# Optimization experiments

Measured on AMD Instinct MI355X. Metric: run time of the kernel, lower is better.

## Reference

```python
import jax, jax.numpy as jnp
import numpy as np

H = 64  # hidden size (fixed by module)

def _gru_cell(x, h, Wih, Whh, bih, bhh):
    # PyTorch GRU cell: gates ordered (r, z, n)
    gi = x @ Wih.T + bih            # [B, 3H]
    gh = h @ Whh.T + bhh            # [B, 3H]
    ir, iz, inn = jnp.split(gi, 3, axis=-1)
    hr, hz, hn = jnp.split(gh, 3, axis=-1)
    r = jax.nn.sigmoid(ir + hr)
    z = jax.nn.sigmoid(iz + hz)
    n = jnp.tanh(inn + r * hn)
    return (1.0 - z) * n + z * h


def setup_inputs() -> dict:
    key = jax.random.key(0)
    ks = jax.random.split(key, 24)
    B, T, NI = 16384, 256, 6
    s = 1.0 / np.sqrt(H)  # torch default GRU init scale
    f32 = jnp.float32
    u = lambda k, shp: jax.random.uniform(k, shp, dtype=f32, minval=-s, maxval=s)
    inp = {
        "x": jax.random.normal(ks[0], (B, T, NI), dtype=f32),
        "target_len": 180,
        # encoder GRU, layer 0 (input size NI) and layer 1 (input size H)
        "e_Wih0": u(ks[1], (3 * H, NI)), "e_Whh0": u(ks[2], (3 * H, H)),
        "e_bih0": u(ks[3], (3 * H,)),    "e_bhh0": u(ks[4], (3 * H,)),
        "e_Wih1": u(ks[5], (3 * H, H)),  "e_Whh1": u(ks[6], (3 * H, H)),
        "e_bih1": u(ks[7], (3 * H,)),    "e_bhh1": u(ks[8], (3 * H,)),
        # decoder GRU, layer 0 (input size 1) and layer 1 (input size H)
        "d_Wih0": u(ks[9], (3 * H, 1)),  "d_Whh0": u(ks[10], (3 * H, H)),
        "d_bih0": u(ks[11], (3 * H,)),   "d_bhh0": u(ks[12], (3 * H,)),
        "d_Wih1": u(ks[13], (3 * H, H)), "d_Whh1": u(ks[14], (3 * H, H)),
        "d_bih1": u(ks[15], (3 * H,)),   "d_bhh1": u(ks[16], (3 * H,)),
        # heads
        "W_on": u(ks[17], (1, H)), "b_on": u(ks[18], (1,)),
        "W_cv": u(ks[19], (1, H)), "b_cv": u(ks[20], (1,)),
    }
    return inp


def reference(x, target_len,
              e_Wih0, e_Whh0, e_bih0, e_bhh0, e_Wih1, e_Whh1, e_bih1, e_bhh1,
              d_Wih0, d_Whh0, d_bih0, d_bhh0, d_Wih1, d_Whh1, d_bih1, d_bhh1,
              W_on, b_on, W_cv, b_cv):
    B = x.shape[0]
    on_threshold = 0.5

    # ---- encoder: 2-layer GRU over the input sequence, keep final hidden ----
    def enc_step(carry, xt):
        h0, h1 = carry
        h0 = _gru_cell(xt, h0, e_Wih0, e_Whh0, e_bih0, e_bhh0)
        h1 = _gru_cell(h0, h1, e_Wih1, e_Whh1, e_bih1, e_bhh1)
        return (h0, h1), None

    h_init = (jnp.zeros((B, H), x.dtype), jnp.zeros((B, H), x.dtype))
    (h0, h1), _ = jax.lax.scan(enc_step, h_init, jnp.swapaxes(x, 0, 1))  # [T,B,NI]

    def dec_step(carry, _):
        prev, h0, h1 = carry                                   # prev: [B,1]
        h0 = _gru_cell(prev, h0, d_Wih0, d_Whh0, d_bih0, d_bhh0)
        h1 = _gru_cell(h0, h1, d_Wih1, d_Whh1, d_bih1, d_bhh1)
        cv = h1 @ W_cv.T + b_cv                                # [B,1]
        logit = h1 @ W_on.T + b_on                             # [B,1]
        gated = (jax.nn.sigmoid(logit) > on_threshold).astype(cv.dtype) * cv
        return (gated, h0, h1), gated

    prev0 = jnp.zeros((B, 1), x.dtype)
    _, outs = jax.lax.scan(dec_step, (prev0, h0, h1), None, length=target_len)
    # outs: [target_len, B, 1] -> [B, target_len, 1] (torch.cat along dim=1)
    return jnp.swapaxes(outs, 0, 1)
```

## Files before the change

### kernel.cpp

```cpp
#include <hip/hip_runtime.h>
#include <math.h>

#define TENC 256
#define NIE  6
#define LH   68
#define WSTR 68

__shared__ float sW1[192 * WSTR];
__shared__ float sU1[192 * WSTR];
__shared__ float sHd[132];
__shared__ float sh0[2][64 * LH];
__shared__ float sh1[64 * LH];

__device__ __forceinline__ float sigm_(float x) {
    return __builtin_amdgcn_rcpf(1.0f + __expf(-x));
}
__device__ __forceinline__ float tanh_(float x) {
    float t = __expf(2.0f * x);
    return (t - 1.0f) * __builtin_amdgcn_rcpf(t + 1.0f);
}

__device__ __forceinline__ void fma4(float& acc, const float4& a, const float4& b) {
    acc = fmaf(a.x, b.x, acc);
    acc = fmaf(a.y, b.y, acc);
    acc = fmaf(a.z, b.z, acc);
    acc = fmaf(a.w, b.w, acc);
}

__device__ __forceinline__ void stage_w1(const float* __restrict__ W1,
                                         const float* __restrict__ U1) {
    for (int s = threadIdx.x; s < 12288; s += 512) {
        int k = s & 63, row = s >> 6;
        int g = row >> 6, j = row & 63;
        int d = (j * 3 + g) * WSTR + k;
        sW1[d] = W1[s];
        sU1[d] = U1[s];
    }
}

template<int KIN>
__device__ __forceinline__ void layer0_c(const float* __restrict__ U0,
                                         const float* w0r, const float* w0z,
                                         const float* w0n,
                                         const float* xin,
                                         const float* b_r, const float* b_z,
                                         const float* b_nx, const float* b_nh,
                                         int jB, int bl,
                                         const float* __restrict__ hb,
                                         float hn[2][4])
{
    float ar[2][4], az[2][4], anx[2][4], anh[2][4];
#pragma unroll
    for (int g = 0; g < 4; ++g) {
#pragma unroll
        for (int jj = 0; jj < 2; ++jj) {
            ar[jj][g] = b_r[jj]; az[jj][g] = b_z[jj];
            anx[jj][g] = b_nx[jj]; anh[jj][g] = b_nh[jj];
        }
    }
#pragma unroll
    for (int jj = 0; jj < 2; ++jj)
#pragma unroll
        for (int g = 0; g < 4; ++g)
#pragma unroll
            for (int k = 0; k < KIN; ++k) {
                ar[jj][g]  = fmaf(w0r[jj * KIN + k], xin[g * KIN + k], ar[jj][g]);
                az[jj][g]  = fmaf(w0z[jj * KIN + k], xin[g * KIN + k], az[jj][g]);
                anx[jj][g] = fmaf(w0n[jj * KIN + k], xin[g * KIN + k], anx[jj][g]);
            }
    const float* u0 = U0 + (size_t)jB * 64;
    const float* u1 = U0 + (size_t)(jB + 1) * 64;
    const float* hr0 = hb + bl * LH;
#pragma unroll 2
    for (int kc = 0; kc < 64; kc += 4) {
        float4 hv[4];
#pragma unroll
        for (int g = 0; g < 4; ++g)
            hv[g] = *(const float4*)(hr0 + g * (16 * LH) + kc);
        float4 r0 = *(const float4*)(u0 + kc);
        float4 z0 = *(const float4*)(u0 + 4096 + kc);
        float4 n0 = *(const float4*)(u0 + 8192 + kc);
        float4 r1 = *(const float4*)(u1 + kc);
        float4 z1 = *(const float4*)(u1 + 4096 + kc);
        float4 n1 = *(const float4*)(u1 + 8192 + kc);
#pragma unroll
        for (int g = 0; g < 4; ++g) {
            fma4(ar[0][g], r0, hv[g]); fma4(az[0][g], z0, hv[g]); fma4(anh[0][g], n0, hv[g]);
            fma4(ar[1][g], r1, hv[g]); fma4(az[1][g], z1, hv[g]); fma4(anh[1][g], n1, hv[g]);
        }
    }
#pragma unroll
    for (int g = 0; g < 4; ++g) {
        float2 ho = *(const float2*)(hb + (bl + 16 * g) * LH + jB);
        float hold[2] = {ho.x, ho.y};
#pragma unroll
        for (int jj = 0; jj < 2; ++jj) {
            float r = sigm_(ar[jj][g]);
            float z = sigm_(az[jj][g]);
            float n = tanh_(fmaf(r, anh[jj][g], anx[jj][g]));
            hn[jj][g] = fmaf(z, hold[jj] - n, n);
        }
    }
}

__device__ __forceinline__ void layer1_c(const float* b_r, const float* b_z,
                                         const float* b_nx, const float* b_nh,
                                         int jB, int bl,
                                         const float* __restrict__ xb,
                                         float hn[2][4])
{
    float ar[2][4], az[2][4], anx[2][4], anh[2][4];
#pragma unroll
    for (int g = 0; g < 4; ++g) {
#pragma unroll
        for (int jj = 0; jj < 2; ++jj) {
            ar[jj][g] = b_r[jj]; az[jj][g] = b_z[jj];
            anx[jj][g] = b_nx[jj]; anh[jj][g] = b_nh[jj];
        }
    }
    const float* wb0 = sW1 + (jB * 3) * WSTR;
    const float* wb1 = sW1 + ((jB + 1) * 3) * WSTR;
    const float* ub0 = sU1 + (jB * 3) * WSTR;
    const float* ub1 = sU1 + ((jB + 1) * 3) * WSTR;
    const float* xr0 = xb + bl * LH;
    const float* hr0 = sh1 + bl * LH;
#pragma unroll 2
    for (int kc = 0; kc < 64; kc += 4) {
        float4 xv[4], hv[4];
#pragma unroll
        for (int g = 0; g < 4; ++g) {
            xv[g] = *(const float4*)(xr0 + g * (16 * LH) + kc);
            hv[g] = *(const float4*)(hr0 + g * (16 * LH) + kc);
        }
        float4 wr0 = *(const float4*)(wb0 + kc);
        float4 wz0 = *(const float4*)(wb0 + WSTR + kc);
        float4 wn0 = *(const float4*)(wb0 + 2 * WSTR + kc);
        float4 ur0 = *(const float4*)(ub0 + kc);
        float4 uz0 = *(const float4*)(ub0 + WSTR + kc);
        float4 un0 = *(const float4*)(ub0 + 2 * WSTR + kc);
        float4 wr1 = *(const float4*)(wb1 + kc);
        float4 wz1 = *(const float4*)(wb1 + WSTR + kc);
        float4 wn1 = *(const float4*)(wb1 + 2 * WSTR + kc);
        float4 ur1 = *(const float4*)(ub1 + kc);
        float4 uz1 = *(const float4*)(ub1 + WSTR + kc);
        float4 un1 = *(const float4*)(ub1 + 2 * WSTR + kc);
#pragma unroll
        for (int g = 0; g < 4; ++g) {
            fma4(ar[0][g], wr0, xv[g]);  fma4(ar[0][g], ur0, hv[g]);
            fma4(az[0][g], wz0, xv[g]);  fma4(az[0][g], uz0, hv[g]);
            fma4(anx[0][g], wn0, xv[g]); fma4(anh[0][g], un0, hv[g]);
            fma4(ar[1][g], wr1, xv[g]);  fma4(ar[1][g], ur1, hv[g]);
            fma4(az[1][g], wz1, xv[g]);  fma4(az[1][g], uz1, hv[g]);
            fma4(anx[1][g], wn1, xv[g]); fma4(anh[1][g], un1, hv[g]);
        }
    }
#pragma unroll
    for (int g = 0; g < 4; ++g) {
        float2 ho = *(const float2*)(sh1 + (bl + 16 * g) * LH + jB);
        float hold[2] = {ho.x, ho.y};
#pragma unroll
        for (int jj = 0; jj < 2; ++jj) {
            float r = sigm_(ar[jj][g]);
            float z = sigm_(az[jj][g]);
            float n = tanh_(fmaf(r, anh[jj][g], anx[jj][g]));
            hn[jj][g] = fmaf(z, hold[jj] - n, n);
        }
    }
}

extern "C" __global__ void __launch_bounds__(512, 2)
ccseq_kernel(const float* __restrict__ x, const int* __restrict__ p_tlen,
             const float* __restrict__ eW0, const float* __restrict__ eU0,
             const float* __restrict__ eBi0, const float* __restrict__ eBh0,
             const float* __restrict__ eW1, const float* __restrict__ eU1,
             const float* __restrict__ eBi1, const float* __restrict__ eBh1,
             const float* __restrict__ dW0, const float* __restrict__ dU0,
             const float* __restrict__ dBi0, const float* __restrict__ dBh0,
             const float* __restrict__ dW1, const float* __restrict__ dU1,
             const float* __restrict__ dBi1, const float* __restrict__ dBh1,
             const float* __restrict__ Won, const float* __restrict__ bon,
             const float* __restrict__ Wcv, const float* __restrict__ bcv,
             float* __restrict__ out)
{
    const int tid  = threadIdx.x;
    const int lane = tid & 63;
    const int wv   = tid >> 6;
    const int jg   = lane >> 4;
    const int bl   = lane & 15;
    const int jB   = wv * 8 + jg * 2;
    const int tlen = p_tlen[0];

    if (tid < 64) { sHd[tid] = Wcv[tid]; sHd[64 + tid] = Won[tid]; }
    for (int i = tid; i < 64 * LH; i += 512) {
        sh0[0][i] = 0.0f; sh0[1][i] = 0.0f; sh1[i] = 0.0f;
    }
    stage_w1(eW1, eU1);
    __syncthreads();

    float w0r[2 * NIE], w0z[2 * NIE], w0n[2 * NIE];
#pragma unroll
    for (int jj = 0; jj < 2; ++jj)
#pragma unroll
        for (int k = 0; k < NIE; ++k) {
            w0r[jj * NIE + k] = eW0[(jB + jj) * NIE + k];
            w0z[jj * NIE + k] = eW0[(64 + jB + jj) * NIE + k];
            w0n[jj * NIE + k] = eW0[(128 + jB + jj) * NIE + k];
        }
    float eb_r[2], eb_z[2], eb_nx[2], eb_nh[2];
    float e1_r[2], e1_z[2], e1_nx[2], e1_nh[2];
#pragma unroll
    for (int jj = 0; jj < 2; ++jj) {
        int j = jB + jj;
        eb_r[jj]  = eBi0[j] + eBh0[j];
        eb_z[jj]  = eBi0[64 + j] + eBh0[64 + j];
        eb_nx[jj] = eBi0[128 + j];
        eb_nh[jj] = eBh0[128 + j];
        e1_r[jj]  = eBi1[j] + eBh1[j];
        e1_z[jj]  = eBi1[64 + j] + eBh1[64 + j];
        e1_nx[jj] = eBi1[128 + j];
        e1_nh[jj] = eBh1[128 + j];
    }

    const size_t bstr = (size_t)TENC * NIE;
    const float* xb[4];
#pragma unroll
    for (int g = 0; g < 4; ++g)
        xb[g] = x + (size_t)(blockIdx.x * 64 + bl + 16 * g) * bstr;

    float xc[4 * NIE], xn[4 * NIE];
#pragma unroll
    for (int g = 0; g < 4; ++g)
#pragma unroll
        for (int k = 0; k < NIE; ++k) xc[g * NIE + k] = xb[g][k];

    int cur = 0;
    for (int t = 0; t < TENC; ++t) {
        const int tn = (t + 1 < TENC) ? (t + 1) : t;
#pragma unroll
        for (int g = 0; g < 4; ++g)
#pragma unroll
            for (int k = 0; k < NIE; ++k) xn[g * NIE + k] = xb[g][tn * NIE + k];

        float hn[2][4];
        layer0_c<NIE>(eU0, w0r, w0z, w0n, xc, eb_r, eb_z, eb_nx, eb_nh,
                      jB, bl, sh0[cur], hn);
#pragma unroll
        for (int g = 0; g < 4; ++g)
            *(float2*)(sh0[cur ^ 1] + (bl + 16 * g) * LH + jB) =
                make_float2(hn[0][g], hn[1][g]);
        __syncthreads();

        layer1_c(e1_r, e1_z, e1_nx, e1_nh, jB, bl, sh0[cur ^ 1], hn);
        __syncthreads();
#pragma unroll
        for (int g = 0; g < 4; ++g)
            *(float2*)(sh1 + (bl + 16 * g) * LH + jB) =
                make_float2(hn[0][g], hn[1][g]);
        __syncthreads();

        cur ^= 1;
#pragma unroll
        for (int i = 0; i < 4 * NIE; ++i) xc[i] = xn[i];
    }

    stage_w1(dW1, dU1);
    float v0r[2], v0z[2], v0n[2];
    float db_r[2], db_z[2], db_nx[2], db_nh[2];
    float d1_r[2], d1_z[2], d1_nx[2], d1_nh[2];
#pragma unroll
    for (int jj = 0; jj < 2; ++jj) {
        int j = jB + jj;
        v0r[jj] = dW0[j]; v0z[jj] = dW0[64 + j]; v0n[jj] = dW0[128 + j];
        db_r[jj]  = dBi0[j] + dBh0[j];
        db_z[jj]  = dBi0[64 + j] + dBh0[64 + j];
        db_nx[jj] = dBi0[128 + j];
        db_nh[jj] = dBh0[128 + j];
        d1_r[jj]  = dBi1[j] + dBh1[j];
        d1_z[jj]  = dBi1[64 + j] + dBh1[64 + j];
        d1_nx[jj] = dBi1[128 + j];
        d1_nh[jj] = dBh1[128 + j];
    }
    const float hbc = bcv[0], hbo = bon[0];
    __syncthreads();

    float prev[4] = {0.0f, 0.0f, 0.0f, 0.0f};
    for (int t = 0; t < tlen; ++t) {
        float hn[2][4];
        layer0_c<1>(dU0, v0r, v0z, v0n, prev, db_r, db_z, db_nx, db_nh,
                    jB, bl, sh0[cur], hn);
#pragma unroll
        for (int g = 0; g < 4; ++g)
            *(float2*)(sh0[cur ^ 1] + (bl + 16 * g) * LH + jB) =
                make_float2(hn[0][g], hn[1][g]);
        __syncthreads();

        layer1_c(d1_r, d1_z, d1_nx, d1_nh, jB, bl, sh0[cur ^ 1], hn);
        __syncthreads();
#pragma unroll
        for (int g = 0; g < 4; ++g)
            *(float2*)(sh1 + (bl + 16 * g) * LH + jB) =
                make_float2(hn[0][g], hn[1][g]);
        __syncthreads();

        float cv[4] = {hbc, hbc, hbc, hbc};
        float lg[4] = {hbo, hbo, hbo, hbo};
        const float* hr0 = sh1 + bl * LH;
#pragma unroll 2
        for (int kc = 0; kc < 64; kc += 4) {
            float4 wc = *(const float4*)(sHd + kc);
            float4 wo = *(const float4*)(sHd + 64 + kc);
#pragma unroll
            for (int g = 0; g < 4; ++g) {
                float4 h4 = *(const float4*)(hr0 + g * (16 * LH) + kc);
                fma4(cv[g], wc, h4);
                fma4(lg[g], wo, h4);
            }
        }
#pragma unroll
        for (int g = 0; g < 4; ++g)
            prev[g] = (lg[g] > 0.0f) ? cv[g] : 0.0f;
        if (tid < 16) {
#pragma unroll
            for (int g = 0; g < 4; ++g)
                out[(size_t)(blockIdx.x * 64 + bl + 16 * g) * tlen + t] = prev[g];
        }
        cur ^= 1;
    }
}

extern "C" void kernel_launch(void* const* d_in, const int* in_sizes, int n_in,
                              void* d_out, int out_size, void* d_ws, size_t ws_size,
                              hipStream_t stream)
{
    (void)n_in; (void)out_size; (void)d_ws; (void)ws_size;
    const float* x    = (const float*)d_in[0];
    const int*   tl   = (const int*)d_in[1];
    const float* eW0  = (const float*)d_in[2];
    const float* eU0  = (const float*)d_in[3];
    const float* eBi0 = (const float*)d_in[4];
    const float* eBh0 = (const float*)d_in[5];
    const float* eW1  = (const float*)d_in[6];
    const float* eU1  = (const float*)d_in[7];
    const float* eBi1 = (const float*)d_in[8];
    const float* eBh1 = (const float*)d_in[9];
    const float* dW0  = (const float*)d_in[10];
    const float* dU0  = (const float*)d_in[11];
    const float* dBi0 = (const float*)d_in[12];
    const float* dBh0 = (const float*)d_in[13];
    const float* dW1  = (const float*)d_in[14];
    const float* dU1  = (const float*)d_in[15];
    const float* dBi1 = (const float*)d_in[16];
    const float* dBh1 = (const float*)d_in[17];
    const float* Won  = (const float*)d_in[18];
    const float* bon  = (const float*)d_in[19];
    const float* Wcv  = (const float*)d_in[20];
    const float* bcv  = (const float*)d_in[21];

    const int B    = in_sizes[0] / (TENC * NIE);
    const int nblk = B / 64;

    ccseq_kernel<<<dim3(nblk), dim3(512), 0, stream>>>(
        x, tl, eW0, eU0, eBi0, eBh0, eW1, eU1, eBi1, eBh1,
        dW0, dU0, dBi0, dBh0, dW1, dU1, dBi1, dBh1,
        Won, bon, Wcv, bcv, (float*)d_out);
}
```

Measured before the change: 8.460 ms.

## Skew encoder layers across timesteps and double-buffer layer-1 hidden state

```diff
diff --git a/kernel.cpp b/kernel.cpp
--- a/kernel.cpp
+++ b/kernel.cpp
@@ -7,10 +7,9 @@
 #define WSTR 68
 
 __shared__ float sW1[192 * WSTR];
-__shared__ float sU1[192 * WSTR];
 __shared__ float sHd[132];
 __shared__ float sh0[2][64 * LH];
-__shared__ float sh1[64 * LH];
+__shared__ float sh1[2][64 * LH];
 
 __device__ __forceinline__ float sigm_(float x) {
     return __builtin_amdgcn_rcpf(1.0f + __expf(-x));
@@ -27,14 +26,11 @@
     acc = fmaf(a.w, b.w, acc);
 }
 
-__device__ __forceinline__ void stage_w1(const float* __restrict__ W1,
-                                         const float* __restrict__ U1) {
+__device__ __forceinline__ void stage_w1(const float* __restrict__ W1) {
     for (int s = threadIdx.x; s < 12288; s += 512) {
         int k = s & 63, row = s >> 6;
         int g = row >> 6, j = row & 63;
-        int d = (j * 3 + g) * WSTR + k;
-        sW1[d] = W1[s];
-        sU1[d] = U1[s];
+        sW1[(j * 3 + g) * WSTR + k] = W1[s];
     }
 }
 
@@ -103,10 +99,12 @@
     }
 }
 
-__device__ __forceinline__ void layer1_c(const float* b_r, const float* b_z,
+__device__ __forceinline__ void layer1_c(const float* __restrict__ U1,
+                                         const float* b_r, const float* b_z,
                                          const float* b_nx, const float* b_nh,
                                          int jB, int bl,
                                          const float* __restrict__ xb,
+                                         const float* __restrict__ hb,
                                          float hn[2][4])
 {
     float ar[2][4], az[2][4], anx[2][4], anh[2][4];
@@ -120,10 +118,10 @@
     }
     const float* wb0 = sW1 + (jB * 3) * WSTR;
     const float* wb1 = sW1 + ((jB + 1) * 3) * WSTR;
-    const float* ub0 = sU1 + (jB * 3) * WSTR;
-    const float* ub1 = sU1 + ((jB + 1) * 3) * WSTR;
+    const float* u0 = U1 + (size_t)jB * 64;
+    const float* u1 = U1 + (size_t)(jB + 1) * 64;
     const float* xr0 = xb + bl * LH;
-    const float* hr0 = sh1 + bl * LH;
+    const float* hr0 = hb + bl * LH;
 #pragma unroll 2
     for (int kc = 0; kc < 64; kc += 4) {
         float4 xv[4], hv[4];
@@ -135,15 +133,15 @@
         float4 wr0 = *(const float4*)(wb0 + kc);
         float4 wz0 = *(const float4*)(wb0 + WSTR + kc);
         float4 wn0 = *(const float4*)(wb0 + 2 * WSTR + kc);
-        float4 ur0 = *(const float4*)(ub0 + kc);
-        float4 uz0 = *(const float4*)(ub0 + WSTR + kc);
-        float4 un0 = *(const float4*)(ub0 + 2 * WSTR + kc);
+        float4 ur0 = *(const float4*)(u0 + kc);
+        float4 uz0 = *(const float4*)(u0 + 4096 + kc);
+        float4 un0 = *(const float4*)(u0 + 8192 + kc);
         float4 wr1 = *(const float4*)(wb1 + kc);
         float4 wz1 = *(const float4*)(wb1 + WSTR + kc);
         float4 wn1 = *(const float4*)(wb1 + 2 * WSTR + kc);
-        float4 ur1 = *(const float4*)(ub1 + kc);
-        float4 uz1 = *(const float4*)(ub1 + WSTR + kc);
-        float4 un1 = *(const float4*)(ub1 + 2 * WSTR + kc);
+        float4 ur1 = *(const float4*)(u1 + kc);
+        float4 uz1 = *(const float4*)(u1 + 4096 + kc);
+        float4 un1 = *(const float4*)(u1 + 8192 + kc);
 #pragma unroll
         for (int g = 0; g < 4; ++g) {
             fma4(ar[0][g], wr0, xv[g]);  fma4(ar[0][g], ur0, hv[g]);
@@ -156,7 +154,7 @@
     }
 #pragma unroll
     for (int g = 0; g < 4; ++g) {
-        float2 ho = *(const float2*)(sh1 + (bl + 16 * g) * LH + jB);
+        float2 ho = *(const float2*)(hb + (bl + 16 * g) * LH + jB);
         float hold[2] = {ho.x, ho.y};
 #pragma unroll
         for (int jj = 0; jj < 2; ++jj) {
@@ -192,9 +190,10 @@
 
     if (tid < 64) { sHd[tid] = Wcv[tid]; sHd[64 + tid] = Won[tid]; }
     for (int i = tid; i < 64 * LH; i += 512) {
-        sh0[0][i] = 0.0f; sh0[1][i] = 0.0f; sh1[i] = 0.0f;
-    }
-    stage_w1(eW1, eU1);
+        sh0[0][i] = 0.0f; sh0[1][i] = 0.0f;
+        sh1[0][i] = 0.0f; sh1[1][i] = 0.0f;
+    }
+    stage_w1(eW1);
     __syncthreads();
 
     float w0r[2 * NIE], w0z[2 * NIE], w0n[2 * NIE];
@@ -228,42 +227,52 @@
         xb[g] = x + (size_t)(blockIdx.x * 64 + bl + 16 * g) * bstr;
 
     float xc[4 * NIE], xn[4 * NIE];
+    float hn[2][4], hn0[2][4];
 #pragma unroll
     for (int g = 0; g < 4; ++g)
 #pragma unroll
         for (int k = 0; k < NIE; ++k) xc[g * NIE + k] = xb[g][k];
 
-    int cur = 0;
+    layer0_c<NIE>(eU0, w0r, w0z, w0n, xc, eb_r, eb_z, eb_nx, eb_nh,
+                  jB, bl, sh0[0], hn);
+#pragma unroll
+    for (int g = 0; g < 4; ++g)
+        *(float2*)(sh0[1] + (bl + 16 * g) * LH + jB) = make_float2(hn[0][g], hn[1][g]);
+#pragma unroll
+    for (int g = 0; g < 4; ++g)
+#pragma unroll
+        for (int k = 0; k < NIE; ++k) xc[g * NIE + k] = xb[g][NIE + k];
+    __syncthreads();
+    int p = 1;
+
     for (int t = 0; t < TENC; ++t) {
-        const int tn = (t + 1 < TENC) ? (t + 1) : t;
+        const int tn = (t + 2 < TENC) ? (t + 2) : (TENC - 1);
 #pragma unroll
         for (int g = 0; g < 4; ++g)
 #pragma unroll
             for (int k = 0; k < NIE; ++k) xn[g * NIE + k] = xb[g][tn * NIE + k];
 
-        float hn[2][4];
-        layer0_c<NIE>(eU0, w0r, w0z, w0n, xc, eb_r, eb_z, eb_nx, eb_nh,
-                      jB, bl, sh0[cur], hn);
-#pragma unroll
-        for (int g = 0; g < 4; ++g)
-            *(float2*)(sh0[cur ^ 1] + (bl + 16 * g) * LH + jB) =
+        layer1_c(eU1, e1_r, e1_z, e1_nx, e1_nh, jB, bl, sh0[p], sh1[p], hn);
+#pragma unroll
+        for (int g = 0; g < 4; ++g)
+            *(float2*)(sh1[p ^ 1] + (bl + 16 * g) * LH + jB) =
                 make_float2(hn[0][g], hn[1][g]);
+
+        if (t + 1 < TENC) {
+            layer0_c<NIE>(eU0, w0r, w0z, w0n, xc, eb_r, eb_z, eb_nx, eb_nh,
+                          jB, bl, sh0[p], hn0);
+#pragma unroll
+            for (int g = 0; g < 4; ++g)
+                *(float2*)(sh0[p ^ 1] + (bl + 16 * g) * LH + jB) =
+                    make_float2(hn0[0][g], hn0[1][g]);
+        }
         __syncthreads();
-
-        layer1_c(e1_r, e1_z, e1_nx, e1_nh, jB, bl, sh0[cur ^ 1], hn);
-        __syncthreads();
-#pragma unroll
-        for (int g = 0; g < 4; ++g)
-            *(float2*)(sh1 + (bl + 16 * g) * LH + jB) =
-                make_float2(hn[0][g], hn[1][g]);
-        __syncthreads();
-
-        cur ^= 1;
+        p ^= 1;
 #pragma unroll
         for (int i = 0; i < 4 * NIE; ++i) xc[i] = xn[i];
     }
 
-    stage_w1(dW1, dU1);
+    stage_w1(dW1);
     float v0r[2], v0z[2], v0n[2];
     float db_r[2], db_z[2], db_nx[2], db_nh[2];
     float d1_r[2], d1_z[2], d1_nx[2], d1_nh[2];
@@ -283,28 +292,30 @@
     const float hbc = bcv[0], hbo = bon[0];
     __syncthreads();
 
+    int p0 = p ^ 1;
+    int p1 = p;
     float prev[4] = {0.0f, 0.0f, 0.0f, 0.0f};
     for (int t = 0; t < tlen; ++t) {
-        float hn[2][4];
         layer0_c<1>(dU0, v0r, v0z, v0n, prev, db_r, db_z, db_nx, db_nh,
-                    jB, bl, sh0[cur], hn);
-#pragma unroll
-        for (int g = 0; g < 4; ++g)
-            *(float2*)(sh0[cur ^ 1] + (bl + 16 * g) * LH + jB) =
+                    jB, bl, sh0[p0], hn);
+#pragma unroll
+        for (int g = 0; g < 4; ++g)
+            *(float2*)(sh0[p0 ^ 1] + (bl + 16 * g) * LH + jB) =
                 make_float2(hn[0][g], hn[1][g]);
         __syncthreads();
-
-        layer1_c(d1_r, d1_z, d1_nx, d1_nh, jB, bl, sh0[cur ^ 1], hn);
-        __syncthreads();
-#pragma unroll
-        for (int g = 0; g < 4; ++g)
-            *(float2*)(sh1 + (bl + 16 * g) * LH + jB) =
+        p0 ^= 1;
+
+        layer1_c(dU1, d1_r, d1_z, d1_nx, d1_nh, jB, bl, sh0[p0], sh1[p1], hn);
+#pragma unroll
+        for (int g = 0; g < 4; ++g)
+            *(float2*)(sh1[p1 ^ 1] + (bl + 16 * g) * LH + jB) =
                 make_float2(hn[0][g], hn[1][g]);
         __syncthreads();
+        p1 ^= 1;
 
         float cv[4] = {hbc, hbc, hbc, hbc};
         float lg[4] = {hbo, hbo, hbo, hbo};
-        const float* hr0 = sh1 + bl * LH;
+        const float* hr0 = sh1[p1] + bl * LH;
 #pragma unroll 2
         for (int kc = 0; kc < 64; kc += 4) {
             float4 wc = *(const float4*)(sHd + kc);
@@ -324,7 +335,6 @@
             for (int g = 0; g < 4; ++g)
                 out[(size_t)(blockIdx.x * 64 + bl + 16 * g) * tlen + t] = prev[g];
         }
-        cur ^= 1;
     }
 }
 
```

Measured after the change: 9.637 ms. 13.9% more time.

## Skew encoder layers across timesteps and rotate triple hidden-state buffers

Applied to the files above, without the earlier changes.

```diff
diff --git a/kernel.cpp b/kernel.cpp
--- a/kernel.cpp
+++ b/kernel.cpp
@@ -9,8 +9,7 @@
 __shared__ float sW1[192 * WSTR];
 __shared__ float sU1[192 * WSTR];
 __shared__ float sHd[132];
-__shared__ float sh0[2][64 * LH];
-__shared__ float sh1[64 * LH];
+__shared__ float shs[3][64 * LH];
 
 __device__ __forceinline__ float sigm_(float x) {
     return __builtin_amdgcn_rcpf(1.0f + __expf(-x));
@@ -107,6 +106,7 @@
                                          const float* b_nx, const float* b_nh,
                                          int jB, int bl,
                                          const float* __restrict__ xb,
+                                         const float* __restrict__ hb,
                                          float hn[2][4])
 {
     float ar[2][4], az[2][4], anx[2][4], anh[2][4];
@@ -123,7 +123,7 @@
     const float* ub0 = sU1 + (jB * 3) * WSTR;
     const float* ub1 = sU1 + ((jB + 1) * 3) * WSTR;
     const float* xr0 = xb + bl * LH;
-    const float* hr0 = sh1 + bl * LH;
+    const float* hr0 = hb + bl * LH;
 #pragma unroll 2
     for (int kc = 0; kc < 64; kc += 4) {
         float4 xv[4], hv[4];
@@ -156,7 +156,7 @@
     }
 #pragma unroll
     for (int g = 0; g < 4; ++g) {
-        float2 ho = *(const float2*)(sh1 + (bl + 16 * g) * LH + jB);
+        float2 ho = *(const float2*)(hb + (bl + 16 * g) * LH + jB);
         float hold[2] = {ho.x, ho.y};
 #pragma unroll
         for (int jj = 0; jj < 2; ++jj) {
@@ -192,7 +192,7 @@
 
     if (tid < 64) { sHd[tid] = Wcv[tid]; sHd[64 + tid] = Won[tid]; }
     for (int i = tid; i < 64 * LH; i += 512) {
-        sh0[0][i] = 0.0f; sh0[1][i] = 0.0f; sh1[i] = 0.0f;
+        shs[0][i] = 0.0f; shs[1][i] = 0.0f; shs[2][i] = 0.0f;
     }
     stage_w1(eW1, eU1);
     __syncthreads();
@@ -227,40 +227,50 @@
     for (int g = 0; g < 4; ++g)
         xb[g] = x + (size_t)(blockIdx.x * 64 + bl + 16 * g) * bstr;
 
-    float xc[4 * NIE], xn[4 * NIE];
+    float xc[4 * NIE];
+    float hn[2][4], hn0[2][4];
 #pragma unroll
     for (int g = 0; g < 4; ++g)
 #pragma unroll
         for (int k = 0; k < NIE; ++k) xc[g * NIE + k] = xb[g][k];
 
-    int cur = 0;
+    layer0_c<NIE>(eU0, w0r, w0z, w0n, xc, eb_r, eb_z, eb_nx, eb_nh,
+                  jB, bl, shs[0] , hn0);
+#pragma unroll
+    for (int g = 0; g < 4; ++g)
+        *(float2*)(shs[1] + (bl + 16 * g) * LH + jB) = make_float2(hn0[0][g], hn0[1][g]);
+    __syncthreads();
+    int ih0 = 1, ih1 = 2, ifr = 0;
+
     for (int t = 0; t < TENC; ++t) {
-        const int tn = (t + 1 < TENC) ? (t + 1) : t;
-#pragma unroll
-        for (int g = 0; g < 4; ++g)
-#pragma unroll
-            for (int k = 0; k < NIE; ++k) xn[g * NIE + k] = xb[g][tn * NIE + k];
-
-        float hn[2][4];
-        layer0_c<NIE>(eU0, w0r, w0z, w0n, xc, eb_r, eb_z, eb_nx, eb_nh,
-                      jB, bl, sh0[cur], hn);
-#pragma unroll
-        for (int g = 0; g < 4; ++g)
-            *(float2*)(sh0[cur ^ 1] + (bl + 16 * g) * LH + jB) =
+        if (t + 1 < TENC) {
+#pragma unroll
+            for (int g = 0; g < 4; ++g)
+#pragma unroll
+                for (int k = 0; k < NIE; ++k)
+                    xc[g * NIE + k] = xb[g][(t + 1) * NIE + k];
+        }
+
+        layer1_c(e1_r, e1_z, e1_nx, e1_nh, jB, bl, shs[ih0], shs[ih1], hn);
+
+        __builtin_amdgcn_sched_barrier(0);
+
+        if (t + 1 < TENC) {
+            layer0_c<NIE>(eU0, w0r, w0z, w0n, xc, eb_r, eb_z, eb_nx, eb_nh,
+                          jB, bl, shs[ih0], hn0);
+#pragma unroll
+            for (int g = 0; g < 4; ++g)
+                *(float2*)(shs[ifr] + (bl + 16 * g) * LH + jB) =
+                    make_float2(hn0[0][g], hn0[1][g]);
+        }
+        __syncthreads();
+#pragma unroll
+        for (int g = 0; g < 4; ++g)
+            *(float2*)(shs[ih1] + (bl + 16 * g) * LH + jB) =
                 make_float2(hn[0][g], hn[1][g]);
         __syncthreads();
 
-        layer1_c(e1_r, e1_z, e1_nx, e1_nh, jB, bl, sh0[cur ^ 1], hn);
-        __syncthreads();
-#pragma unroll
-        for (int g = 0; g < 4; ++g)
-            *(float2*)(sh1 + (bl + 16 * g) * LH + jB) =
-                make_float2(hn[0][g], hn[1][g]);
-        __syncthreads();
-
-        cur ^= 1;
-#pragma unroll
-        for (int i = 0; i < 4 * NIE; ++i) xc[i] = xn[i];
+        if (t + 1 < TENC) { int o = ih0; ih0 = ifr; ifr = o; }
     }
 
     stage_w1(dW1, dU1);
@@ -285,26 +295,24 @@
 
     float prev[4] = {0.0f, 0.0f, 0.0f, 0.0f};
     for (int t = 0; t < tlen; ++t) {
-        float hn[2][4];
         layer0_c<1>(dU0, v0r, v0z, v0n, prev, db_r, db_z, db_nx, db_nh,
-                    jB, bl, sh0[cur], hn);
-#pragma unroll
-        for (int g = 0; g < 4; ++g)
-            *(float2*)(sh0[cur ^ 1] + (bl + 16 * g) * LH + jB) =
+                    jB, bl, shs[ih0], hn);
+#pragma unroll
+        for (int g = 0; g < 4; ++g)
+            *(float2*)(shs[ifr] + (bl + 16 * g) * LH + jB) =
                 make_float2(hn[0][g], hn[1][g]);
         __syncthreads();
 
-        layer1_c(d1_r, d1_z, d1_nx, d1_nh, jB, bl, sh0[cur ^ 1], hn);
-        __syncthreads();
-#pragma unroll
-        for (int g = 0; g < 4; ++g)
-            *(float2*)(sh1 + (bl + 16 * g) * LH + jB) =
+        layer1_c(d1_r, d1_z, d1_nx, d1_nh, jB, bl, shs[ifr], shs[ih1], hn);
+#pragma unroll
+        for (int g = 0; g < 4; ++g)
+            *(float2*)(shs[ih0] + (bl + 16 * g) * LH + jB) =
                 make_float2(hn[0][g], hn[1][g]);
         __syncthreads();
 
         float cv[4] = {hbc, hbc, hbc, hbc};
         float lg[4] = {hbo, hbo, hbo, hbo};
-        const float* hr0 = sh1 + bl * LH;
+        const float* hr0 = shs[ih0] + bl * LH;
 #pragma unroll 2
         for (int kc = 0; kc < 64; kc += 4) {
             float4 wc = *(const float4*)(sHd + kc);
@@ -324,7 +332,8 @@
             for (int g = 0; g < 4; ++g)
                 out[(size_t)(blockIdx.x * 64 + bl + 16 * g) * tlen + t] = prev[g];
         }
-        cur ^= 1;
+        int o0 = ih0, o1 = ih1;
+        ih0 = ifr; ih1 = o0; ifr = o1;
     }
 }
 
```

After: 8.472 ms. No clear change (+0.1%).
